# Kernel tuning notes

Hardware: AMD Instinct MI355X
Metric: run time of the kernel (lower is better)

Reference implementation:

```python
import jax, jax.numpy as jnp
import numpy as np

ALPHA = 0.1
EPS = 1e-8


def _segment_mean_std(feats, idx, num_segments):
    # feats: (N, C), idx: (N,) int -> mean/std per segment, torch.std is unbiased (ddof=1)
    ones = jnp.ones((feats.shape[0],), feats.dtype)
    cnt = jax.ops.segment_sum(ones, idx, num_segments=num_segments)  # (B,)
    ssum = jax.ops.segment_sum(feats, idx, num_segments=num_segments)  # (B, C)
    mean = ssum / cnt[:, None]
    diff = feats - mean[idx]
    var = jax.ops.segment_sum(diff * diff, idx, num_segments=num_segments) / (cnt[:, None] - 1.0)
    std = jnp.sqrt(jnp.maximum(var, 0.0)) + EPS
    return mean, std


def _adain(content_feats, style_feats, content_batch_indices, style_batch_indices, num_batches):
    c_mean, c_std = _segment_mean_std(content_feats, content_batch_indices, num_batches)
    s_mean, s_std = _segment_mean_std(style_feats, style_batch_indices, num_batches)
    # sequential EMA of global stats across batch ids (globals start as first batch's style stats)
    g0 = jnp.concatenate([s_mean[:1], s_std[:1]], axis=0)  # (2, C)
    rest = jnp.stack([s_mean[1:], s_std[1:]], axis=1)  # (B-1, 2, C)

    def step(g, s):
        g_new = (1.0 - ALPHA) * g + ALPHA * s
        return g_new, g_new

    _, g_rest = jax.lax.scan(step, g0, rest)
    g_all = jnp.concatenate([g0[None], g_rest], axis=0)  # (B, 2, C)
    g_mean, g_std = g_all[:, 0], g_all[:, 1]  # (B, C) each
    # per-row gather + normalize (each batch uses globals AFTER its own update)
    ci = content_batch_indices
    return g_std[ci] * (content_feats - c_mean[ci]) / c_std[ci] + g_mean[ci]


def setup_inputs() -> dict:
    key = jax.random.key(0)
    k1, k2, k3, k4 = jax.random.split(key, 4)
    N_c, N_s, C, B = 1000000, 250000, 64, 16
    return {
        "content_feats": jax.random.normal(k1, (N_c, C), dtype=jnp.float32),
        "style_feats": jax.random.normal(k2, (N_s, C), dtype=jnp.float32),
        "content_batch_indices": jax.random.randint(k3, (N_c,), 0, B, dtype=jnp.int32),
        "style_batch_indices": jax.random.randint(k4, (N_s,), 0, B, dtype=jnp.int32),
        "num_batches": B,
    }


def reference(content_feats, style_feats, content_batch_indices, style_batch_indices, num_batches):
    return _adain(content_feats, style_feats, content_batch_indices, style_batch_indices, num_batches)
```

## Files before the change

kernel.cpp:

```cpp
#include <hip/hip_runtime.h>


#define NB 16
#define NC 64
#define NREP 16
#define CBLKS 1638
#define SBLKS 410

typedef float fvec4 __attribute__((ext_vector_type(4)));
typedef float f32x4 __attribute__((ext_vector_type(4)));
typedef short bf16x8 __attribute__((ext_vector_type(8)));

#define WS_CPART 0
#define WS_SPART (NREP * 2048)
#define WS_CCNT  (2 * NREP * 2048)
#define WS_SCNT  (WS_CCNT + NREP * NB)
#define WS_SCALE (WS_SCNT + NREP * NB)
#define WS_BIAS  (WS_SCALE + 1024)
#define WS_ZERO_FLOATS WS_SCALE

__device__ __forceinline__ unsigned cvtpk(float lo, float hi)
{
    unsigned r;
    asm("v_cvt_pk_bf16_f32 %0, %1, %2" : "=v"(r) : "v"(lo), "v"(hi));
    return r;
}

__device__ __forceinline__ void gload16(const float* g, float* l)
{
    __builtin_amdgcn_global_load_lds(
        (const __attribute__((address_space(1))) void*)g,
        (__attribute__((address_space(3))) void*)l, 16, 0, 0);
}

__device__ __forceinline__ void reduce_body(
    const float* __restrict__ feats, const int* __restrict__ idx, int nrows,
    float* __restrict__ part, float* __restrict__ cntp,
    int blk, int nblk, int tid, float* buf , float* lsum )
{
    const int lane = tid & 63;
    const int wv   = tid >> 6;
    const int half = lane >> 4;
    const int sub  = lane & 15;

    const int ntiles = (nrows + 31) >> 5;
    const int tpb = (ntiles + nblk - 1) / nblk;
    const int t0 = blk * tpb;
    const int t1 = (t0 + tpb < ntiles) ? (t0 + tpb) : ntiles;

    f32x4 accS = {0, 0, 0, 0}, accQ = {0, 0, 0, 0};
    int cnti = 0;

    const int i0 = 2 * wv, i1 = 2 * wv + 1;
    const int srow0 = i0 * 4 + (sub >> 2) * 0 + (lane >> 4);
    const int scol  = (lane & 15) * 4;

    int vidx_next = -1;
    if (t0 < t1) {
        const int rl = (t0 << 5) + (lane & 31);
        vidx_next = (rl < nrows) ? idx[rl] : -1;
        {
            const int rb = t0 << 5;
            int ra = rb + i0 * 4 + (lane >> 4); if (ra > nrows - 1) ra = nrows - 1;
            int rbx = rb + i1 * 4 + (lane >> 4); if (rbx > nrows - 1) rbx = nrows - 1;
            gload16(feats + (size_t)ra * NC + (lane & 15) * 4, buf + i0 * 256);
            gload16(feats + (size_t)rbx * NC + (lane & 15) * 4, buf + i1 * 256);
        }
    }

    for (int t = t0; t < t1; ++t) {
        __syncthreads();
        const int vidx = vidx_next;

        if (t + 1 < t1) {
            const int rl = ((t + 1) << 5) + (lane & 31);
            vidx_next = (rl < nrows) ? idx[rl] : -1;
        }

        if (wv == 0) {
            #pragma unroll
            for (int b = 0; b < NB; ++b) {
                const unsigned long long m = __ballot(vidx == b) & 0xFFFFFFFFull;
                cnti += (lane == b) ? (int)__popcll(m) : 0;
            }
        }

        union { unsigned w[4]; bf16x8 v; } A;
        const int kb4 = half * 32;
        #pragma unroll
        for (int i = 0; i < 4; ++i) {
            const int k0 = __builtin_amdgcn_ds_bpermute(kb4 + 8 * i,     vidx);
            const int k1 = __builtin_amdgcn_ds_bpermute(kb4 + 8 * i + 4, vidx);
            const unsigned lo = (k0 == sub) ? 0x3F80u     : 0u;
            const unsigned hi = (k1 == sub) ? 0x3F800000u : 0u;
            A.w[i] = lo | hi;
        }

        float xv[8];
        #pragma unroll
        for (int j = 0; j < 8; ++j)
            xv[j] = buf[(half * 8 + j) * NC + wv * 16 + sub];

        union { unsigned w[4]; bf16x8 v; } Bs, Bq;
        #pragma unroll
        for (int i = 0; i < 4; ++i) {
            const float a0 = xv[2 * i], a1 = xv[2 * i + 1];
            Bs.w[i] = cvtpk(a0, a1);
            Bq.w[i] = cvtpk(a0 * a0, a1 * a1);
        }

        __syncthreads();

        if (t + 1 < t1) {
            const int rb = (t + 1) << 5;
            int ra = rb + i0 * 4 + (lane >> 4); if (ra > nrows - 1) ra = nrows - 1;
            int rbx = rb + i1 * 4 + (lane >> 4); if (rbx > nrows - 1) rbx = nrows - 1;
            gload16(feats + (size_t)ra * NC + (lane & 15) * 4, buf + i0 * 256);
            gload16(feats + (size_t)rbx * NC + (lane & 15) * 4, buf + i1 * 256);
        }

        accS = __builtin_amdgcn_mfma_f32_16x16x32_bf16(A.v, Bs.v, accS, 0, 0, 0);
        accQ = __builtin_amdgcn_mfma_f32_16x16x32_bf16(A.v, Bq.v, accQ, 0, 0, 0);
    }

    #pragma unroll
    for (int i = 0; i < 4; ++i) {
        const int m = half * 4 + i;
        lsum[m * NC + wv * 16 + sub]        = accS[i];
        lsum[1024 + m * NC + wv * 16 + sub] = accQ[i];
    }
    __syncthreads();
    float* dst = part + (blk & (NREP - 1)) * 2048;
    for (int i = tid; i < 2048; i += 256)
        atomicAdd(&dst[i], lsum[i]);
    if (wv == 0 && lane < NB)
        atomicAdd(&cntp[(blk & (NREP - 1)) * NB + lane], (float)cnti);
}

__global__ __launch_bounds__(256) void reduce_stats(
    const float* __restrict__ content, const int* __restrict__ ci, int Nc,
    const float* __restrict__ style,   const int* __restrict__ si, int Ns,
    float* __restrict__ ws)
{
    __shared__ float buf[2048];
    __shared__ float lsum[2048];
    if (blockIdx.x < CBLKS)
        reduce_body(content, ci, Nc, ws + WS_CPART, ws + WS_CCNT,
                    blockIdx.x, CBLKS, threadIdx.x, buf, lsum);
    else
        reduce_body(style, si, Ns, ws + WS_SPART, ws + WS_SCNT,
                    blockIdx.x - CBLKS, SBLKS, threadIdx.x, buf, lsum);
}

__global__ void finalize_kernel(float* __restrict__ ws)
{
    if (threadIdx.x >= NC) return;
    const int c = threadIdx.x;
    const float* c_part = ws + WS_CPART;
    const float* s_part = ws + WS_SPART;
    const float* c_cntp = ws + WS_CCNT;
    const float* s_cntp = ws + WS_SCNT;
    float* scale = ws + WS_SCALE;
    float* bias  = ws + WS_BIAS;

    float gm = 0.f, gs = 0.f;
    for (int b = 0; b < NB; ++b) {
        float csum = 0.f, csq = 0.f, ssum = 0.f, ssq = 0.f, ccnt = 0.f, scnt = 0.f;
        #pragma unroll
        for (int rep = 0; rep < NREP; ++rep) {
            csum += c_part[rep * 2048 + b * NC + c];
            csq  += c_part[rep * 2048 + 1024 + b * NC + c];
            ssum += s_part[rep * 2048 + b * NC + c];
            ssq  += s_part[rep * 2048 + 1024 + b * NC + c];
            ccnt += c_cntp[rep * NB + b];
            scnt += s_cntp[rep * NB + b];
        }
        const float smean = ssum / scnt;
        const float svar  = (ssq - scnt * smean * smean) / (scnt - 1.0f);
        const float sstd  = sqrtf(fmaxf(svar, 0.f)) + 1e-8f;
        if (b == 0) { gm = smean; gs = sstd; }
        else        { gm = 0.9f * gm + 0.1f * smean; gs = 0.9f * gs + 0.1f * sstd; }
        const float cmean = csum / ccnt;
        const float cvar  = (csq - ccnt * cmean * cmean) / (ccnt - 1.0f);
        const float cstd  = sqrtf(fmaxf(cvar, 0.f)) + 1e-8f;
        const float sc = gs / cstd;
        scale[b * NC + c] = sc;
        bias [b * NC + c] = gm - sc * cmean;
    }
}

__global__ __launch_bounds__(256) void apply_kernel(
    const float* __restrict__ content, const int* __restrict__ ci, int Nc,
    const float* __restrict__ ws, fvec4* __restrict__ out4)
{
    __shared__ fvec4 s_sc[NB * 17];
    __shared__ fvec4 s_bi[NB * 17];
    const fvec4* scale4 = (const fvec4*)(ws + WS_SCALE);
    const fvec4* bias4  = (const fvec4*)(ws + WS_BIAS);
    for (int i = threadIdx.x; i < NB * 16; i += 256) {
        const int b = i >> 4, c4 = i & 15;
        s_sc[b * 17 + c4] = scale4[i];
        s_bi[b * 17 + c4] = bias4[i];
    }
    __syncthreads();

    const fvec4* feats4 = (const fvec4*)content;
    const int total4 = Nc * 16;
    const int stride = gridDim.x * 256;
    for (int i = blockIdx.x * 256 + threadIdx.x; i < total4; i += stride) {
        const int r  = i >> 4;
        const int c4 = i & 15;
        const int b  = ci[r];
        const fvec4 v  = feats4[i];
        const fvec4 sc = s_sc[b * 17 + c4];
        const fvec4 bi = s_bi[b * 17 + c4];
        fvec4 o;
        o.x = fmaf(sc.x, v.x, bi.x);
        o.y = fmaf(sc.y, v.y, bi.y);
        o.z = fmaf(sc.z, v.z, bi.z);
        o.w = fmaf(sc.w, v.w, bi.w);
        __builtin_nontemporal_store(o, &out4[i]);
    }
}

extern "C" void kernel_launch(void* const* d_in, const int* in_sizes, int n_in,
                              void* d_out, int out_size, void* d_ws, size_t ws_size,
                              hipStream_t stream)
{
    const float* content = (const float*)d_in[0];
    const float* style   = (const float*)d_in[1];
    const int*   ci      = (const int*)d_in[2];
    const int*   si      = (const int*)d_in[3];

    const int Nc = in_sizes[0] / NC;
    const int Ns = in_sizes[1] / NC;

    float* ws = (float*)d_ws;
    (void)hipMemsetAsync(ws, 0, WS_ZERO_FLOATS * sizeof(float), stream);

    reduce_stats<<<CBLKS + SBLKS, 256, 0, stream>>>(content, ci, Nc, style, si, Ns, ws);
    finalize_kernel<<<1, 64, 0, stream>>>(ws);
    apply_kernel<<<2048, 256, 0, stream>>>(content, ci, Nc, ws, (fvec4*)d_out);
}
```

Before: 186.4 us.

## Double-buffer LDS tile staging in reduce kernel with XOR-swizzled columns

Replaces the single LDS staging buffer with two ping-pong buffers, so the next tile's global-to-LDS load is issued right after the loop-top barrier and the second barrier per iteration is dropped. Column chunks are XOR-swizzled on store and read to reduce LDS bank conflicts. Block counts for the content and style reductions are also reduced. This doubles the staging LDS per block, which can lower occupancy, and relies on the single remaining barrier to order buffer reuse correctly.

```diff
diff --git a/kernel.cpp b/kernel.cpp
--- a/kernel.cpp
+++ b/kernel.cpp
@@ -4,8 +4,8 @@
 #define NB 16
 #define NC 64
 #define NREP 16
-#define CBLKS 1638
-#define SBLKS 410
+#define CBLKS 1228
+#define SBLKS 308
 
 typedef float fvec4 __attribute__((ext_vector_type(4)));
 typedef float f32x4 __attribute__((ext_vector_type(4)));
@@ -33,6 +33,20 @@
         (__attribute__((address_space(3))) void*)l, 16, 0, 0);
 }
 
+__device__ __forceinline__ void stage_tile(
+    const float* __restrict__ feats, int nrows, int rb, int wv, int lane,
+    float* bufp)
+{
+    #pragma unroll
+    for (int u = 0; u < 2; ++u) {
+        const int i = 2 * wv + u;
+        int rg = rb + i * 4 + (lane >> 4);
+        if (rg > nrows - 1) rg = nrows - 1;
+        const int c4 = (lane & 15) ^ (2 * ((i >> 1) & 3));
+        gload16(feats + (size_t)rg * NC + c4 * 4, bufp + i * 256);
+    }
+}
+
 __device__ __forceinline__ void reduce_body(
     const float* __restrict__ feats, const int* __restrict__ idx, int nrows,
     float* __restrict__ part, float* __restrict__ cntp,
@@ -43,38 +57,34 @@
     const int half = lane >> 4;
     const int sub  = lane & 15;
 
+    f32x4 accS = {0, 0, 0, 0}, accQ = {0, 0, 0, 0};
+    int cnti = 0;
+
     const int ntiles = (nrows + 31) >> 5;
     const int tpb = (ntiles + nblk - 1) / nblk;
     const int t0 = blk * tpb;
     const int t1 = (t0 + tpb < ntiles) ? (t0 + tpb) : ntiles;
 
-    f32x4 accS = {0, 0, 0, 0}, accQ = {0, 0, 0, 0};
-    int cnti = 0;
-
-    const int i0 = 2 * wv, i1 = 2 * wv + 1;
-    const int srow0 = i0 * 4 + (sub >> 2) * 0 + (lane >> 4);
-    const int scol  = (lane & 15) * 4;
-
-    int vidx_next = -1;
+    const int c4p   = (wv * 4 + (sub >> 2)) ^ (2 * half);
+    const int rbase = half * 8 * NC + c4p * 4 + (sub & 3);
+
+    int vidx = -1;
     if (t0 < t1) {
+        stage_tile(feats, nrows, t0 << 5, wv, lane, buf);
         const int rl = (t0 << 5) + (lane & 31);
-        vidx_next = (rl < nrows) ? idx[rl] : -1;
-        {
-            const int rb = t0 << 5;
-            int ra = rb + i0 * 4 + (lane >> 4); if (ra > nrows - 1) ra = nrows - 1;
-            int rbx = rb + i1 * 4 + (lane >> 4); if (rbx > nrows - 1) rbx = nrows - 1;
-            gload16(feats + (size_t)ra * NC + (lane & 15) * 4, buf + i0 * 256);
-            gload16(feats + (size_t)rbx * NC + (lane & 15) * 4, buf + i1 * 256);
-        }
-    }
-
+        vidx = (rl < nrows) ? idx[rl] : -1;
+    }
+
+    int cur = 0;
     for (int t = t0; t < t1; ++t) {
         __syncthreads();
-        const int vidx = vidx_next;
-
+
+        if (t + 1 < t1)
+            stage_tile(feats, nrows, (t + 1) << 5, wv, lane, buf + (cur ^ 1) * 2048);
+        int vn = -1;
         if (t + 1 < t1) {
             const int rl = ((t + 1) << 5) + (lane & 31);
-            vidx_next = (rl < nrows) ? idx[rl] : -1;
+            vn = (rl < nrows) ? idx[rl] : -1;
         }
 
         if (wv == 0) {
@@ -96,10 +106,11 @@
             A.w[i] = lo | hi;
         }
 
+        const float* bp = buf + cur * 2048;
         float xv[8];
         #pragma unroll
         for (int j = 0; j < 8; ++j)
-            xv[j] = buf[(half * 8 + j) * NC + wv * 16 + sub];
+            xv[j] = bp[rbase + j * NC];
 
         union { unsigned w[4]; bf16x8 v; } Bs, Bq;
         #pragma unroll
@@ -109,18 +120,11 @@
             Bq.w[i] = cvtpk(a0 * a0, a1 * a1);
         }
 
-        __syncthreads();
-
-        if (t + 1 < t1) {
-            const int rb = (t + 1) << 5;
-            int ra = rb + i0 * 4 + (lane >> 4); if (ra > nrows - 1) ra = nrows - 1;
-            int rbx = rb + i1 * 4 + (lane >> 4); if (rbx > nrows - 1) rbx = nrows - 1;
-            gload16(feats + (size_t)ra * NC + (lane & 15) * 4, buf + i0 * 256);
-            gload16(feats + (size_t)rbx * NC + (lane & 15) * 4, buf + i1 * 256);
-        }
-
         accS = __builtin_amdgcn_mfma_f32_16x16x32_bf16(A.v, Bs.v, accS, 0, 0, 0);
         accQ = __builtin_amdgcn_mfma_f32_16x16x32_bf16(A.v, Bq.v, accQ, 0, 0, 0);
+
+        vidx = vn;
+        cur ^= 1;
     }
 
     #pragma unroll
@@ -142,7 +146,7 @@
     const float* __restrict__ style,   const int* __restrict__ si, int Ns,
     float* __restrict__ ws)
 {
-    __shared__ float buf[2048];
+    __shared__ float buf[2 * 2048];
     __shared__ float lsum[2048];
     if (blockIdx.x < CBLKS)
         reduce_body(content, ci, Nc, ws + WS_CPART, ws + WS_CCNT,
```

Result: faster. 182.3 us, median of 2 (-2.2%).
